# Optimization experiments

Hardware: AMD Instinct MI355X
Metric: run time of the kernel (lower is better)

Reference implementation:

```python
import math
import jax, jax.numpy as jnp
import numpy as np

B, P, L = 32, 128, 64
DIN, TE, H, NH, NL = 16, 64, 512, 8, 2
DH = H // NH
DP = DIN + TE
TAU = 300.0
DELTA = 300.0

_PARAM_SPEC = [
    ("te_scale_w", (1, 1)), ("te_scale_b", (1,)),
    ("te_per_w", (TE - 1, 1)), ("te_per_b", (TE - 1,)),
    ("inp_w", (H, DP)), ("inp_b", (H,)),
    ("wq", (H, H)), ("bq", (H,)), ("wk", (H, H)), ("bk", (H,)),
    ("wv", (H, H)), ("bv", (H,)), ("wo", (H, H)), ("bo", (H,)),
    ("ffn_w1", (H, H)), ("ffn_b1", (H,)), ("ffn_w2", (H, H)), ("ffn_b2", (H,)),
    ("ln1_g", (H,)), ("ln1_b", (H,)), ("ln2_g", (H,)), ("ln2_b", (H,)),
    ("exists_bias", (1, 1, H)),
    ("gwq", (NL, H, H)), ("gbq", (NL, H)), ("gwk", (NL, H, H)), ("gbk", (NL, H)),
    ("gwv", (NL, H, H)), ("gbv", (NL, H)), ("gwo", (NL, H, H)), ("gbo", (NL, H)),
]


def setup_inputs() -> dict:
    key = jax.random.key(0)
    ks = jax.random.split(key, 3 + len(_PARAM_SPEC))
    inp = {
        "x": jax.random.normal(ks[0], (B, P, L, DIN), jnp.float32),
        "tt": jax.random.uniform(ks[1], (B, P, L, 1), jnp.float32),
        "mask": jax.random.randint(ks[2], (B, P, L, 1), 0, 2).astype(jnp.int32),
    }
    for i, (name, shp) in enumerate(_PARAM_SPEC):
        inp[name] = 0.02 * jax.random.normal(ks[3 + i], shp, jnp.float32)
    # LayerNorm affine params: gamma=1, beta=0
    inp["ln1_g"] = jnp.ones((H,), jnp.float32)
    inp["ln1_b"] = jnp.zeros((H,), jnp.float32)
    inp["ln2_g"] = jnp.ones((H,), jnp.float32)
    inp["ln2_b"] = jnp.zeros((H,), jnp.float32)
    return inp


def _layernorm(x, g, b, eps=1e-5):
    m = x.mean(-1, keepdims=True)
    v = ((x - m) ** 2).mean(-1, keepdims=True)
    return (x - m) / jnp.sqrt(v + eps) * g + b


def _time_bias(m):
    idx = jnp.arange(m)
    dist = jnp.abs(idx[:, None] - idx[None, :]).astype(jnp.float32) * DELTA
    return jnp.log(jnp.exp(-dist / TAU) + 1e-12)  # [P, P]


def _pos_encoding(p, d):
    pos = jnp.arange(p, dtype=jnp.float32)[:, None]
    div = jnp.exp(jnp.arange(0, d, 2, dtype=jnp.float32) * (-math.log(10000.0) / d))
    pe = jnp.zeros((p, d), jnp.float32)
    pe = pe.at[:, 0::2].set(jnp.sin(pos * div))
    pe = pe.at[:, 1::2].set(jnp.cos(pos * div))
    return pe


def reference(x, tt, mask,
              te_scale_w, te_scale_b, te_per_w, te_per_b,
              inp_w, inp_b, wq, bq, wk, bk, wv, bv, wo, bo,
              ffn_w1, ffn_b1, ffn_w2, ffn_b2, ln1_g, ln1_b, ln2_g, ln2_b,
              exists_bias, gwq, gbq, gwk, gbk, gwv, gbv, gwo, gbo):
    b, p, l, _ = x.shape
    # --- Learnable time embedding: scale linear + sin(periodic linear), concat ---
    te1 = tt @ te_scale_w.T + te_scale_b                      # [B,P,L,1]
    te2 = jnp.sin(tt @ te_per_w.T + te_per_b)                 # [B,P,L,TE-1]
    pts = jnp.concatenate([x, te1, te2], axis=-1)             # [B,P,L,DP]

    valid = (mask[..., 0] > 0).reshape(b * p, l)              # [N,L] bool
    h = (pts.reshape(b * p, l, DP) @ inp_w.T) + inp_b         # [N,L,H]

    has_any = jnp.any(valid, axis=1)                          # [N]
    key_pad = ~valid
    # Empty patches: unmask position 0 and zero its features
    key_pad = key_pad.at[:, 0].set(key_pad[:, 0] & has_any)
    pos0 = (jnp.arange(l) == 0)[None, :, None]
    h = jnp.where((~has_any)[:, None, None] & pos0, 0.0, h)

    # --- Intra-patch MHA (GAT) ---
    def heads(t, w, bias):
        return ((t @ w.T) + bias).reshape(b * p, l, NH, DH)
    q, k, v = heads(h, wq, bq), heads(h, wk, bk), heads(h, wv, bv)
    sc = jnp.einsum("nqhd,nkhd->nhqk", q, k) / math.sqrt(DH)
    sc = jnp.where(key_pad[:, None, None, :], -1e9, sc)
    z = jnp.einsum("nhqk,nkhd->nqhd", jax.nn.softmax(sc, axis=-1), v)
    z = z.reshape(b * p, l, H) @ wo.T + bo
    h = _layernorm(h + z, ln1_g, ln1_b)
    ffn = jax.nn.relu(h @ ffn_w1.T + ffn_b1) @ ffn_w2.T + ffn_b2
    h = _layernorm(h + ffn, ln2_g, ln2_b)

    # Masked mean pooling -> patch tokens
    w = valid.astype(jnp.float32)[..., None]                  # [N,L,1]
    denom = jnp.clip(w.sum(axis=1), 1.0)
    h = ((h * w).sum(axis=1) / denom).reshape(b, p, H)        # [B,P,H]

    # Exists bias for missing patches + positional encoding
    pexists = has_any.reshape(b, p).astype(jnp.float32)       # [B,P]
    h = h + exists_bias * (1.0 - pexists)[..., None]
    h = h + _pos_encoding(p, H)[None]

    # --- Patch-level time-biased graph attention stack (residual) ---
    tb = _time_bias(p)[None, None]                            # [1,1,P,P]
    kp = (pexists <= 0.0)[:, None, None, :]                   # [B,1,1,P]
    for li in range(NL):
        def gh(t, w, bias):
            return ((t @ w.T) + bias).reshape(b, p, NH, DH)
        q = gh(h, gwq[li], gbq[li])
        k = gh(h, gwk[li], gbk[li])
        v = gh(h, gwv[li], gbv[li])
        att = jnp.einsum("bqhd,bkhd->bhqk", q, k) / math.sqrt(DH) + tb
        att = jnp.where(kp, -1e9, att)
        out = jnp.einsum("bhqk,bkhd->bqhd", jax.nn.softmax(att, axis=-1), v)
        out = out.reshape(b, p, H) @ gwo[li].T + gbo[li]
        out = out * pexists[..., None]
        h = h + out
    return h
```

## Files before the change

kernel.cpp:

```cpp
#include <hip/hip_runtime.h>

#define NTOK 4096
#define CH   512
#define NCHUNK 8

typedef _Float16 f16;
typedef __attribute__((ext_vector_type(8))) _Float16 half8;
typedef __attribute__((ext_vector_type(4))) _Float16 half4;
typedef __attribute__((ext_vector_type(4))) float f32x4;

#define OFF_INPW 0
#define OFF_WQKV (512*128)
#define OFF_WO   (OFF_WQKV + 3*512*512)
#define OFF_W1   (OFF_WO + 512*512)
#define OFF_W2   (OFF_W1 + 512*512)
#define OFF_GW   (OFF_W2 + 512*512)
#define WBF_TOT  (OFF_GW + 8*512*512)

static __device__ __forceinline__ f32x4 mfma16(half8 a, half8 b, f32x4 c){
  return __builtin_amdgcn_mfma_f32_16x16x32_f16(a, b, c, 0, 0, 0);
}

static __device__ __forceinline__ void gld_lds16(const f16* g, f16* l){
  __builtin_amdgcn_global_load_lds(
      (const __attribute__((address_space(1))) void*)g,
      (__attribute__((address_space(3))) void*)l, 16, 0, 0);
}

__global__ __launch_bounds__(256) void conv_weights(
    const float* __restrict__ inpw, const float* __restrict__ wq, const float* __restrict__ wk,
    const float* __restrict__ wv, const float* __restrict__ wo, const float* __restrict__ w1,
    const float* __restrict__ w2, const float* __restrict__ gwq, const float* __restrict__ gwk,
    const float* __restrict__ gwv, const float* __restrict__ gwo, f16* __restrict__ wbf,
    const float* __restrict__ bq, const float* __restrict__ bk, const float* __restrict__ bv,
    const float* __restrict__ gbq, const float* __restrict__ gbk, const float* __restrict__ gbv,
    float* __restrict__ biasb)
{
  int e = blockIdx.x*256 + threadIdx.x;
  int y = blockIdx.y;
  if (y == 0){
    if (e < 512*128){
      int row = e>>7, col = e&127;
      float v = (col < 80) ? inpw[row*80 + col] : 0.f;
      wbf[OFF_INPW + e] = (f16)v;
    }
    return;
  }
  if (y == 15){
    if (e < 1536){
      biasb[e] = (e < 512) ? bq[e] : (e < 1024 ? bk[e-512] : bv[e-1024]);
    } else if (e < 3*1536){
      int idx = e - 1536, li = idx/1536, c = idx - li*1536;
      float v = (c < 512) ? gbq[li*512 + c] : (c < 1024 ? gbk[li*512 + c-512] : gbv[li*512 + c-1024]);
      biasb[e] = v;
    }
    return;
  }
  if (e >= 512*512) return;
  const float* src; int off;
  if (y <= 6){
    const float* tab[6] = {wq, wk, wv, wo, w1, w2};
    src = tab[y-1]; off = OFF_WQKV + (y-1)*512*512;
  } else {
    int idx = y-7; int li = idx>>2, part = idx&3;
    const float* tab[4] = {gwq, gwk, gwv, gwo};
    src = tab[part] + (size_t)li*512*512; off = OFF_GW + idx*512*512;
  }
  wbf[off + e] = (f16)src[e];
}

__global__ __launch_bounds__(256) void build_mask(
    const int* __restrict__ mask, float* __restrict__ mb, float* __restrict__ pex)
{
  int wv = threadIdx.x>>6, lane = threadIdx.x&63;
  int n = blockIdx.x*4 + wv;
  int valid = mask[(size_t)n*64 + lane] > 0;
  unsigned long long ball = __ballot(valid);
  int hasany = (ball != 0ull);
  int masked = (lane == 0) ? (!valid && hasany) : (!valid);
  mb[(size_t)n*64 + lane] = masked ? -1e9f : 0.f;
  if (lane == 0) pex[n] = hasany ? 1.f : 0.f;
}

__global__ __launch_bounds__(256) void pts_build(
    const float* __restrict__ x, const float* __restrict__ tt,
    const float* __restrict__ tsw, const float* __restrict__ tsb,
    const float* __restrict__ tpw, const float* __restrict__ tpb,
    f16* __restrict__ pts, int rowbase)
{
  int e = blockIdx.x*256 + threadIdx.x;
  int r = e>>7, col = e&127;
  size_t grow = (size_t)rowbase + r;
  float v;
  if (col < 16) v = x[grow*16 + col];
  else if (col >= 80) v = 0.f;
  else {
    float t = tt[grow];
    if (col == 16) v = t*tsw[0] + tsb[0];
    else           v = __sinf(t*tpw[col-17] + tpb[col-17]);
  }
  pts[e] = (f16)v;
}

template<int RESID, bool RELU, bool OUTF32, bool ZEMPTY>
__global__ __launch_bounds__(256) void gemm128(
    const f16* __restrict__ A, const f16* __restrict__ W, const float* __restrict__ bias,
    void* __restrict__ Cout, const void* __restrict__ Rsd, const float* __restrict__ pex,
    int K, int lda, int ldc, int nbase)
{
  __shared__ __align__(16) f16 As[128][64];
  __shared__ __align__(16) f16 Bs[128][64];
  const int tid = threadIdx.x;
  const int m0 = blockIdx.x*128, n0 = blockIdx.y*128;
  const int wv = tid>>6, lane = tid&63, l15 = lane&15, quad = lane>>4;
  const int wm = (wv&1)*64, wn = (wv>>1)*64;
  const int srow = lane>>3;
  const int schunk = (lane&7) ^ srow;
  f32x4 acc[4][4] = {};
  for (int kc = 0; kc < K; kc += 64){
    __syncthreads();
    #pragma unroll
    for (int i=0; i<4; i++){
      const int rA = wv*32 + i*8;
      gld_lds16(A + (size_t)(m0 + rA + srow)*lda + kc + schunk*8, &As[rA][0]);
      gld_lds16(W + (size_t)(n0 + rA + srow)*K   + kc + schunk*8, &Bs[rA][0]);
    }
    __syncthreads();
    #pragma unroll
    for (int kk=0; kk<2; kk++){
      half8 av[4], bv8[4];
      #pragma unroll
      for (int t=0; t<4; t++){
        const int ra = wm + t*16 + l15;
        av[t]  = *(const half8*)(&As[ra][(((kk*4 + quad) ^ (ra&7)))*8]);
        const int rb = wn + t*16 + l15;
        bv8[t] = *(const half8*)(&Bs[rb][(((kk*4 + quad) ^ (rb&7)))*8]);
      }
      #pragma unroll
      for (int mt=0; mt<4; mt++)
        #pragma unroll
        for (int nt=0; nt<4; nt++)
          acc[mt][nt] = mfma16(av[mt], bv8[nt], acc[mt][nt]);
    }
  }
  #pragma unroll
  for (int mt=0; mt<4; mt++){
    #pragma unroll
    for (int nt=0; nt<4; nt++){
      #pragma unroll
      for (int i=0; i<4; i++){
        int gr = m0 + wm + mt*16 + quad*4 + i;
        int gc = n0 + wn + nt*16 + l15;
        float v = acc[mt][nt][i] + bias[gc];
        if (RELU) v = fmaxf(v, 0.f);
        if (RESID == 1) v += (float)((const f16*)Rsd)[(size_t)gr*ldc + gc];
        if (ZEMPTY){ if ((gr&63)==0 && pex[nbase + (gr>>6)]==0.f) v = 0.f; }
        if (RESID == 2) v = v*pex[gr] + ((const float*)Rsd)[(size_t)gr*ldc + gc];
        if (OUTF32) ((float*)Cout)[(size_t)gr*ldc + gc] = v;
        else        ((f16*)Cout)[(size_t)gr*ldc + gc] = (f16)v;
      }
    }
  }
}

__global__ __launch_bounds__(128) void attn_patch(
    f16* __restrict__ qkv, const float* __restrict__ maskbias, int nbase)
{
  __shared__ f16 Vt[2][64][72];
  __shared__ f16 Ps[2][64][72];
  __shared__ float mbs[64];
  const int tid = threadIdx.x, wv = tid>>6, lane = tid&63, l15 = lane&15, quad = lane>>4;
  const int n = blockIdx.x, h = blockIdx.y*2 + wv;
  if (tid < 64) mbs[tid] = maskbias[(size_t)(nbase+n)*64 + tid];
  const f16* Vb = qkv + 1024 + h*64;
  for (int i=0; i<64; i++)
    Vt[wv][lane][i] = Vb[((size_t)n*64 + i)*1536 + lane];
  __syncthreads();
  const f16* Qb  = qkv + (size_t)n*64*1536 + h*64;
  const f16* Kbb = Qb + 512;
  f32x4 sacc[4][4] = {};
  #pragma unroll
  for (int kc=0; kc<2; kc++){
    half8 af[4], bf[4];
    #pragma unroll
    for (int t4=0; t4<4; t4++){
      af[t4] = *(const half8*)(Qb  + (size_t)(t4*16 + l15)*1536 + kc*32 + quad*8);
      bf[t4] = *(const half8*)(Kbb + (size_t)(t4*16 + l15)*1536 + kc*32 + quad*8);
    }
    #pragma unroll
    for (int ti=0; ti<4; ti++)
      #pragma unroll
      for (int tj=0; tj<4; tj++)
        sacc[ti][tj] = mfma16(af[ti], bf[tj], sacc[ti][tj]);
  }
  #pragma unroll
  for (int ti=0; ti<4; ti++){
    #pragma unroll
    for (int i=0; i<4; i++){
      float mx = -1e30f;
      #pragma unroll
      for (int tj=0; tj<4; tj++){
        float sv = sacc[ti][tj][i]*0.125f + mbs[tj*16 + l15];
        sacc[ti][tj][i] = sv;
        mx = fmaxf(mx, sv);
      }
      #pragma unroll
      for (int off=1; off<16; off<<=1) mx = fmaxf(mx, __shfl_xor(mx, off, 64));
      float sum = 0.f;
      #pragma unroll
      for (int tj=0; tj<4; tj++){
        float pv = __expf(sacc[ti][tj][i] - mx);
        sacc[ti][tj][i] = pv; sum += pv;
      }
      #pragma unroll
      for (int off=1; off<16; off<<=1) sum += __shfl_xor(sum, off, 64);
      float inv = 1.f/sum;
      int q = ti*16 + quad*4 + i;
      #pragma unroll
      for (int tj=0; tj<4; tj++)
        Ps[wv][q][tj*16 + l15] = (f16)(sacc[ti][tj][i]*inv);
    }
  }
  __syncthreads();
  f32x4 zacc[4][4] = {};
  #pragma unroll
  for (int kc=0; kc<2; kc++){
    half8 va[4], pb[4];
    #pragma unroll
    for (int t4=0; t4<4; t4++){
      va[t4] = *(const half8*)(&Vt[wv][t4*16 + l15][kc*32 + quad*8]);
      pb[t4] = *(const half8*)(&Ps[wv][t4*16 + l15][kc*32 + quad*8]);
    }
    #pragma unroll
    for (int ti2=0; ti2<4; ti2++)
      #pragma unroll
      for (int tj=0; tj<4; tj++)
        zacc[ti2][tj] = mfma16(va[ti2], pb[tj], zacc[ti2][tj]);
  }
  __syncthreads();
  #pragma unroll
  for (int ti2=0; ti2<4; ti2++)
    #pragma unroll
    for (int tj=0; tj<4; tj++){
      int q = tj*16 + l15, d0 = ti2*16 + quad*4;
      half4 pk;
      #pragma unroll
      for (int i=0; i<4; i++) pk[i] = (f16)zacc[ti2][tj][i];
      *(half4*)(&Vt[wv][q][d0]) = pk;
    }
  __syncthreads();
  #pragma unroll
  for (int i=0; i<8; i++){
    int q = i*8 + (lane>>3), d0 = (lane&7)*8;
    *(uint4*)(qkv + ((size_t)n*64 + q)*1536 + h*64 + d0) = *(const uint4*)(&Vt[wv][q][d0]);
  }
}

__global__ __launch_bounds__(256) void ln_rows(
    const f16* __restrict__ X, f16* __restrict__ Y,
    const float* __restrict__ g, const float* __restrict__ b)
{
  int wv = threadIdx.x>>6, lane = threadIdx.x&63;
  size_t row = (size_t)blockIdx.x*4 + wv;
  half8 raw = *(const half8*)(X + row*512 + lane*8);
  float xv[8];
  #pragma unroll
  for (int j=0; j<8; j++) xv[j] = (float)raw[j];
  float s = 0.f;
  #pragma unroll
  for (int j=0; j<8; j++) s += xv[j];
  #pragma unroll
  for (int off=1; off<64; off<<=1) s += __shfl_xor(s, off, 64);
  float mean = s*(1.f/512.f);
  float vs = 0.f;
  #pragma unroll
  for (int j=0; j<8; j++){ float d = xv[j]-mean; vs += d*d; }
  #pragma unroll
  for (int off=1; off<64; off<<=1) vs += __shfl_xor(vs, off, 64);
  float rstd = rsqrtf(vs*(1.f/512.f) + 1e-5f);
  half8 o;
  #pragma unroll
  for (int j=0; j<8; j++){
    int c = lane*8 + j;
    o[j] = (f16)((xv[j]-mean)*rstd*g[c] + b[c]);
  }
  *(half8*)(Y + row*512 + lane*8) = o;
}

__global__ __launch_bounds__(256) void pool_ln2(
    const f16* __restrict__ X, const int* __restrict__ mask,
    const float* __restrict__ g, const float* __restrict__ b, const float* __restrict__ eb,
    float* __restrict__ out, int nbase)
{
  __shared__ float mArr[64], rArr[64], vArr[64];
  const int tid = threadIdx.x, wv = tid>>6, lane = tid&63;
  const int n = blockIdx.x, ng = nbase + n, p = ng & 127;
  for (int j=0; j<16; j++){
    int l = wv*16 + j;
    half8 raw = *(const half8*)(X + ((size_t)n*64 + l)*512 + lane*8);
    float s=0.f, ss=0.f;
    #pragma unroll
    for (int jj=0; jj<8; jj++){ float f = (float)raw[jj]; s += f; ss += f*f; }
    #pragma unroll
    for (int off=1; off<64; off<<=1){ s += __shfl_xor(s, off, 64); ss += __shfl_xor(ss, off, 64); }
    if (lane == 0){
      float m = s*(1.f/512.f);
      mArr[l] = m; rArr[l] = rsqrtf(ss*(1.f/512.f) - m*m + 1e-5f);
    }
  }
  if (tid < 64) vArr[tid] = (mask[(size_t)ng*64 + tid] > 0) ? 1.f : 0.f;
  __syncthreads();
  float cnt = 0.f;
  #pragma unroll
  for (int l=0; l<64; l++) cnt += vArr[l];
  float denom = fmaxf(cnt, 1.f);
  float pexv = cnt > 0.f ? 1.f : 0.f;
  float a0=0.f, a1=0.f;
  for (int l=0; l<64; l++){
    float wgt = vArr[l], m = mArr[l], rs = rArr[l];
    float x0 = (float)X[((size_t)n*64+l)*512 + tid];
    float x1 = (float)X[((size_t)n*64+l)*512 + tid + 256];
    a0 += wgt*(x0-m)*rs; a1 += wgt*(x1-m)*rs;
  }
  #pragma unroll
  for (int k=0; k<2; k++){
    int c = tid + k*256;
    float acc = k ? a1 : a0;
    float fr = __expf(-(float)(c & ~1) * (9.210340371976184f/512.f));
    float ang = (float)p * fr;
    float pe = (c & 1) ? cosf(ang) : sinf(ang);
    float o = (g[c]*acc + b[c]*cnt)/denom + eb[c]*(1.f - pexv) + pe;
    out[(size_t)ng*512 + c] = o;
  }
}

__global__ __launch_bounds__(256) void cvt_f32_f16(const float* __restrict__ s, f16* __restrict__ d){
  int i = blockIdx.x*256 + threadIdx.x;
  d[i] = (f16)s[i];
}

__global__ __launch_bounds__(256) void attn_graph(
    f16* __restrict__ qkv, const float* __restrict__ pexists)
{
  __shared__ f16 Vt[64][136];
  __shared__ f16 Ps[4][32][136];
  __shared__ float pxs[128];
  const int tid = threadIdx.x, wv = tid>>6, lane = tid&63, l15 = lane&15, quad = lane>>4;
  const int b = blockIdx.x, h = blockIdx.y;
  if (tid < 128) pxs[tid] = pexists[b*128 + tid];
  const f16* Vb = qkv + 1024 + h*64;
  for (int i=0; i<32; i++){
    int e = tid + i*256, k = e>>6, d = e&63;
    Vt[d][k] = Vb[((size_t)b*128 + k)*1536 + d];
  }
  __syncthreads();
  const f16* Qb = qkv + h*64;
  const f16* Kb = qkv + 512 + h*64;
  const int qb = wv*32;
  f32x4 sacc[2][8] = {};
  #pragma unroll
  for (int kc=0; kc<2; kc++){
    half8 af[2], bf[8];
    #pragma unroll
    for (int ti=0; ti<2; ti++)
      af[ti] = *(const half8*)(Qb + ((size_t)b*128 + qb + ti*16 + l15)*1536 + kc*32 + quad*8);
    #pragma unroll
    for (int tj=0; tj<8; tj++)
      bf[tj] = *(const half8*)(Kb + ((size_t)b*128 + tj*16 + l15)*1536 + kc*32 + quad*8);
    #pragma unroll
    for (int ti=0; ti<2; ti++)
      #pragma unroll
      for (int tj=0; tj<8; tj++)
        sacc[ti][tj] = mfma16(af[ti], bf[tj], sacc[ti][tj]);
  }
  #pragma unroll
  for (int ti=0; ti<2; ti++){
    #pragma unroll
    for (int i=0; i<4; i++){
      int q = qb + ti*16 + quad*4 + i;
      float mx = -1e30f;
      #pragma unroll
      for (int tj=0; tj<8; tj++){
        int col = tj*16 + l15;
        int dd = q - col; if (dd < 0) dd = -dd;
        float tb = __logf(__expf(-(float)dd) + 1e-12f);
        float sv = sacc[ti][tj][i]*0.125f + tb + (pxs[col] > 0.f ? 0.f : -1e9f);
        sacc[ti][tj][i] = sv;
        mx = fmaxf(mx, sv);
      }
      #pragma unroll
      for (int off=1; off<16; off<<=1) mx = fmaxf(mx, __shfl_xor(mx, off, 64));
      float sum = 0.f;
      #pragma unroll
      for (int tj=0; tj<8; tj++){
        float pv = __expf(sacc[ti][tj][i] - mx);
        sacc[ti][tj][i] = pv; sum += pv;
      }
      #pragma unroll
      for (int off=1; off<16; off<<=1) sum += __shfl_xor(sum, off, 64);
      float inv = 1.f/sum;
      int ql = ti*16 + quad*4 + i;
      #pragma unroll
      for (int tj=0; tj<8; tj++)
        Ps[wv][ql][tj*16 + l15] = (f16)(sacc[ti][tj][i]*inv);
    }
  }
  __syncthreads();
  f32x4 zacc[4][2] = {};
  #pragma unroll
  for (int kc=0; kc<4; kc++){
    half8 va[4], pb[2];
    #pragma unroll
    for (int ti2=0; ti2<4; ti2++)
      va[ti2] = *(const half8*)(&Vt[ti2*16 + l15][kc*32 + quad*8]);
    #pragma unroll
    for (int tjq=0; tjq<2; tjq++)
      pb[tjq] = *(const half8*)(&Ps[wv][tjq*16 + l15][kc*32 + quad*8]);
    #pragma unroll
    for (int ti2=0; ti2<4; ti2++)
      #pragma unroll
      for (int tjq=0; tjq<2; tjq++)
        zacc[ti2][tjq] = mfma16(va[ti2], pb[tjq], zacc[ti2][tjq]);
  }
  __syncthreads();
  #pragma unroll
  for (int ti2=0; ti2<4; ti2++)
    #pragma unroll
    for (int tjq=0; tjq<2; tjq++){
      int ql = tjq*16 + l15, d0 = ti2*16 + quad*4;
      half4 pk;
      #pragma unroll
      for (int i=0; i<4; i++) pk[i] = (f16)zacc[ti2][tjq][i];
      *(half4*)(&Ps[wv][ql][d0]) = pk;
    }
  __syncthreads();
  {
    int q = tid>>1, hf = tid&1;
    const f16* src = &Ps[q>>5][q&31][hf*32];
    #pragma unroll
    for (int j=0; j<4; j++)
      *(uint4*)(qkv + ((size_t)b*128 + q)*1536 + h*64 + hf*32 + j*8) = *(const uint4*)(src + j*8);
  }
}

extern "C" void kernel_launch(void* const* d_in, const int* in_sizes, int n_in,
                              void* d_out, int out_size, void* d_ws, size_t ws_size,
                              hipStream_t stream)
{
  (void)in_sizes; (void)n_in; (void)out_size; (void)ws_size;
  const float* x    = (const float*)d_in[0];
  const float* tt   = (const float*)d_in[1];
  const int*   mask = (const int*)  d_in[2];
  const float* tsw  = (const float*)d_in[3];
  const float* tsb  = (const float*)d_in[4];
  const float* tpw  = (const float*)d_in[5];
  const float* tpb  = (const float*)d_in[6];
  const float* inpw = (const float*)d_in[7];
  const float* inpb = (const float*)d_in[8];
  const float* wq   = (const float*)d_in[9];
  const float* bq   = (const float*)d_in[10];
  const float* wk   = (const float*)d_in[11];
  const float* bk   = (const float*)d_in[12];
  const float* wv   = (const float*)d_in[13];
  const float* bv   = (const float*)d_in[14];
  const float* wo   = (const float*)d_in[15];
  const float* bo   = (const float*)d_in[16];
  const float* w1   = (const float*)d_in[17];
  const float* b1   = (const float*)d_in[18];
  const float* w2   = (const float*)d_in[19];
  const float* b2   = (const float*)d_in[20];
  const float* ln1g = (const float*)d_in[21];
  const float* ln1b = (const float*)d_in[22];
  const float* ln2g = (const float*)d_in[23];
  const float* ln2b = (const float*)d_in[24];
  const float* eb   = (const float*)d_in[25];
  const float* gwq  = (const float*)d_in[26];
  const float* gbq  = (const float*)d_in[27];
  const float* gwk  = (const float*)d_in[28];
  const float* gbk  = (const float*)d_in[29];
  const float* gwv  = (const float*)d_in[30];
  const float* gbv  = (const float*)d_in[31];
  const float* gwo  = (const float*)d_in[32];
  const float* gbo  = (const float*)d_in[33];
  float* out = (float*)d_out;

  char* wp = (char*)d_ws;
  auto alloc = [&](size_t bytes)->char*{
    char* p = wp; wp += (bytes + 255) & ~(size_t)255; return p;
  };
  f16*   wbf   = (f16*)  alloc((size_t)WBF_TOT*2);
  float* mb    = (float*)alloc((size_t)NTOK*64*4);
  float* pex   = (float*)alloc((size_t)NTOK*4);
  float* biasb = (float*)alloc((size_t)3*1536*4);
  f16*   ptsb  = (f16*)  alloc((size_t)CH*64*128*2);
  f16*   bufA  = (f16*)  alloc((size_t)CH*64*512*2);
  f16*   bufB  = (f16*)  alloc((size_t)CH*64*512*2);
  f16*   bufC  = (f16*)  alloc((size_t)CH*64*512*2);
  f16*   qkv   = (f16*)  alloc((size_t)CH*64*1536*2);

  conv_weights<<<dim3(1024,16),256,0,stream>>>(inpw,wq,wk,wv,wo,w1,w2,gwq,gwk,gwv,gwo,wbf,
                                               bq,bk,bv,gbq,gbk,gbv,biasb);
  build_mask<<<NTOK/4,256,0,stream>>>(mask, mb, pex);

  const int MB = CH*64/128;
  for (int ch=0; ch<NCHUNK; ch++){
    int nbase = ch*CH;
    int rowbase = nbase*64;
    pts_build<<<CH*64*128/256,256,0,stream>>>(x,tt,tsw,tsb,tpw,tpb,ptsb,rowbase);
    gemm128<0,false,false,true ><<<dim3(MB,4),256,0,stream>>>(ptsb, wbf+OFF_INPW, inpb, bufA, nullptr, pex, 128, 128, 512, nbase);
    gemm128<0,false,false,false><<<dim3(MB,12),256,0,stream>>>(bufA, wbf+OFF_WQKV, biasb, qkv, nullptr, nullptr, 512, 512, 1536, 0);
    attn_patch<<<dim3(CH,4),128,0,stream>>>(qkv, mb, nbase);
    gemm128<1,false,false,false><<<dim3(MB,4),256,0,stream>>>(qkv, wbf+OFF_WO, bo, bufA, bufA, nullptr, 512, 1536, 512, 0);
    ln_rows<<<CH*64/4,256,0,stream>>>(bufA, bufB, ln1g, ln1b);
    gemm128<0,true ,false,false><<<dim3(MB,4),256,0,stream>>>(bufB, wbf+OFF_W1, b1, bufC, nullptr, nullptr, 512, 512, 512, 0);
    gemm128<1,false,false,false><<<dim3(MB,4),256,0,stream>>>(bufC, wbf+OFF_W2, b2, bufB, bufB, nullptr, 512, 512, 512, 0);
    pool_ln2<<<CH,256,0,stream>>>(bufB, mask, ln2g, ln2b, eb, out, nbase);
  }

  f16* hbf  = bufA;
  f16* qkvg = bufB;
  for (int li=0; li<2; li++){
    cvt_f32_f16<<<NTOK*512/256,256,0,stream>>>(out, hbf);
    gemm128<0,false,false,false><<<dim3(32,12),256,0,stream>>>(hbf, wbf+OFF_GW + (size_t)li*4*512*512, biasb + 1536*(1+li), qkvg, nullptr, nullptr, 512, 512, 1536, 0);
    attn_graph<<<dim3(32,8),256,0,stream>>>(qkvg, pex);
    gemm128<2,false,true ,false><<<dim3(32,4),256,0,stream>>>(qkvg, wbf+OFF_GW + (size_t)(li*4+3)*512*512, gbo+li*512, out, out, pex, 512, 1536, 512, 0);
  }
}
```

Baseline: 2.398 ms.

## Double-buffer GEMM staging, vectorize epilogue via LDS, fuse f16 conversions

The GEMM now double-buffers its LDS tiles, issuing the next K-slice's global-to-LDS loads before computing the current one. Its epilogue stages results through shared memory so that output, residual and pex handling use 16-byte vector accesses. attn_patch loads V with half8 vector reads before transposing it. The standalone f32-to-f16 conversion kernels are removed: pool_ln2 and the first graph output GEMM now write an f16 copy of h directly. Risks include an extra f16 rounding of values before the residual add in the epilogue and higher LDS use per block.

```diff
diff --git a/kernel.cpp b/kernel.cpp
--- a/kernel.cpp
+++ b/kernel.cpp
@@ -102,14 +102,16 @@
   pts[e] = (f16)v;
 }
 
-template<int RESID, bool RELU, bool OUTF32, bool ZEMPTY>
+template<int RESID, bool RELU, bool OUTF32, bool ZEMPTY, bool DUAL>
 __global__ __launch_bounds__(256) void gemm128(
     const f16* __restrict__ A, const f16* __restrict__ W, const float* __restrict__ bias,
     void* __restrict__ Cout, const void* __restrict__ Rsd, const float* __restrict__ pex,
-    int K, int lda, int ldc, int nbase)
-{
-  __shared__ __align__(16) f16 As[128][64];
-  __shared__ __align__(16) f16 Bs[128][64];
+    f16* __restrict__ Cdual, int K, int lda, int ldc, int nbase)
+{
+  __shared__ union {
+    f16 stg[2][2][128][64];
+    f16 cs[128][136];
+  } sm;
   const int tid = threadIdx.x;
   const int m0 = blockIdx.x*128, n0 = blockIdx.y*128;
   const int wv = tid>>6, lane = tid&63, l15 = lane&15, quad = lane>>4;
@@ -117,24 +119,30 @@
   const int srow = lane>>3;
   const int schunk = (lane&7) ^ srow;
   f32x4 acc[4][4] = {};
-  for (int kc = 0; kc < K; kc += 64){
-    __syncthreads();
+
+  auto stage = [&](int kc, int b){
     #pragma unroll
     for (int i=0; i<4; i++){
       const int rA = wv*32 + i*8;
-      gld_lds16(A + (size_t)(m0 + rA + srow)*lda + kc + schunk*8, &As[rA][0]);
-      gld_lds16(W + (size_t)(n0 + rA + srow)*K   + kc + schunk*8, &Bs[rA][0]);
-    }
+      gld_lds16(A + (size_t)(m0 + rA + srow)*lda + kc + schunk*8, &sm.stg[b][0][rA][0]);
+      gld_lds16(W + (size_t)(n0 + rA + srow)*K   + kc + schunk*8, &sm.stg[b][1][rA][0]);
+    }
+  };
+
+  stage(0, 0);
+  int buf = 0;
+  for (int kc = 0; kc < K; kc += 64, buf ^= 1){
     __syncthreads();
+    if (kc + 64 < K) stage(kc + 64, buf^1);
     #pragma unroll
     for (int kk=0; kk<2; kk++){
       half8 av[4], bv8[4];
       #pragma unroll
       for (int t=0; t<4; t++){
         const int ra = wm + t*16 + l15;
-        av[t]  = *(const half8*)(&As[ra][(((kk*4 + quad) ^ (ra&7)))*8]);
+        av[t]  = *(const half8*)(&sm.stg[buf][0][ra][(((kk*4 + quad) ^ (ra&7)))*8]);
         const int rb = wn + t*16 + l15;
-        bv8[t] = *(const half8*)(&Bs[rb][(((kk*4 + quad) ^ (rb&7)))*8]);
+        bv8[t] = *(const half8*)(&sm.stg[buf][1][rb][(((kk*4 + quad) ^ (rb&7)))*8]);
       }
       #pragma unroll
       for (int mt=0; mt<4; mt++)
@@ -143,22 +151,62 @@
           acc[mt][nt] = mfma16(av[mt], bv8[nt], acc[mt][nt]);
     }
   }
-  #pragma unroll
-  for (int mt=0; mt<4; mt++){
-    #pragma unroll
-    for (int nt=0; nt<4; nt++){
+  __syncthreads();
+  #pragma unroll
+  for (int nt=0; nt<4; nt++){
+    const float bz = bias[n0 + wn + nt*16 + l15];
+    #pragma unroll
+    for (int mt=0; mt<4; mt++){
       #pragma unroll
       for (int i=0; i<4; i++){
-        int gr = m0 + wm + mt*16 + quad*4 + i;
-        int gc = n0 + wn + nt*16 + l15;
-        float v = acc[mt][nt][i] + bias[gc];
+        float v = acc[mt][nt][i] + bz;
         if (RELU) v = fmaxf(v, 0.f);
-        if (RESID == 1) v += (float)((const f16*)Rsd)[(size_t)gr*ldc + gc];
-        if (ZEMPTY){ if ((gr&63)==0 && pex[nbase + (gr>>6)]==0.f) v = 0.f; }
-        if (RESID == 2) v = v*pex[gr] + ((const float*)Rsd)[(size_t)gr*ldc + gc];
-        if (OUTF32) ((float*)Cout)[(size_t)gr*ldc + gc] = v;
-        else        ((f16*)Cout)[(size_t)gr*ldc + gc] = (f16)v;
+        sm.cs[wm + mt*16 + quad*4 + i][wn + nt*16 + l15] = (f16)v;
       }
+    }
+  }
+  __syncthreads();
+  const int row = tid>>1, c0 = (tid&1)*64;
+  const int gr = m0 + row;
+  float rowscale = 1.f;
+  bool zrow = false;
+  if (ZEMPTY) zrow = ((gr&63)==0) && (pex[nbase + (gr>>6)] == 0.f);
+  if (RESID == 2) rowscale = pex[gr];
+  #pragma unroll
+  for (int j=0; j<8; j++){
+    const int gc = n0 + c0 + j*8;
+    half8 hv = *(const half8*)(&sm.cs[row][c0 + j*8]);
+    float fv[8];
+    #pragma unroll
+    for (int u=0; u<8; u++) fv[u] = (float)hv[u];
+    if (RESID == 1){
+      half8 rv = *(const half8*)((const f16*)Rsd + (size_t)gr*ldc + gc);
+      #pragma unroll
+      for (int u=0; u<8; u++) fv[u] += (float)rv[u];
+    }
+    if (RESID == 2){
+      #pragma unroll
+      for (int u=0; u<8; u++)
+        fv[u] = fv[u]*rowscale + ((const float*)Rsd)[(size_t)gr*ldc + gc + u];
+    }
+    if (ZEMPTY && zrow){
+      #pragma unroll
+      for (int u=0; u<8; u++) fv[u] = 0.f;
+    }
+    if (OUTF32){
+      #pragma unroll
+      for (int u=0; u<8; u++) ((float*)Cout)[(size_t)gr*ldc + gc + u] = fv[u];
+    } else {
+      half8 ov;
+      #pragma unroll
+      for (int u=0; u<8; u++) ov[u] = (f16)fv[u];
+      *(half8*)((f16*)Cout + (size_t)gr*ldc + gc) = ov;
+    }
+    if (DUAL){
+      half8 ov;
+      #pragma unroll
+      for (int u=0; u<8; u++) ov[u] = (f16)fv[u];
+      *(half8*)(Cdual + (size_t)gr*512 + gc) = ov;
     }
   }
 }
@@ -172,9 +220,14 @@
   const int tid = threadIdx.x, wv = tid>>6, lane = tid&63, l15 = lane&15, quad = lane>>4;
   const int n = blockIdx.x, h = blockIdx.y*2 + wv;
   if (tid < 64) mbs[tid] = maskbias[(size_t)(nbase+n)*64 + tid];
-  const f16* Vb = qkv + 1024 + h*64;
-  for (int i=0; i<64; i++)
-    Vt[wv][lane][i] = Vb[((size_t)n*64 + i)*1536 + lane];
+  const f16* Vbp = qkv + (size_t)n*64*1536 + 1024 + h*64;
+  #pragma unroll
+  for (int i=0; i<8; i++){
+    int key = i*8 + (lane>>3), d0 = (lane&7)*8;
+    half8 vv = *(const half8*)(Vbp + (size_t)key*1536 + d0);
+    #pragma unroll
+    for (int j=0; j<8; j++) Vt[wv][d0+j][key] = vv[j];
+  }
   __syncthreads();
   const f16* Qb  = qkv + (size_t)n*64*1536 + h*64;
   const f16* Kbb = Qb + 512;
@@ -290,7 +343,7 @@
 __global__ __launch_bounds__(256) void pool_ln2(
     const f16* __restrict__ X, const int* __restrict__ mask,
     const float* __restrict__ g, const float* __restrict__ b, const float* __restrict__ eb,
-    float* __restrict__ out, int nbase)
+    float* __restrict__ out, f16* __restrict__ hb, int nbase)
 {
   __shared__ float mArr[64], rArr[64], vArr[64];
   const int tid = threadIdx.x, wv = tid>>6, lane = tid&63;
@@ -331,12 +384,8 @@
     float pe = (c & 1) ? cosf(ang) : sinf(ang);
     float o = (g[c]*acc + b[c]*cnt)/denom + eb[c]*(1.f - pexv) + pe;
     out[(size_t)ng*512 + c] = o;
-  }
-}
-
-__global__ __launch_bounds__(256) void cvt_f32_f16(const float* __restrict__ s, f16* __restrict__ d){
-  int i = blockIdx.x*256 + threadIdx.x;
-  d[i] = (f16)s[i];
+    hb[(size_t)ng*512 + c] = (f16)o;
+  }
 }
 
 __global__ __launch_bounds__(256) void attn_graph(
@@ -492,6 +541,7 @@
   float* mb    = (float*)alloc((size_t)NTOK*64*4);
   float* pex   = (float*)alloc((size_t)NTOK*4);
   float* biasb = (float*)alloc((size_t)3*1536*4);
+  f16*   hbf   = (f16*)  alloc((size_t)NTOK*512*2);
   f16*   ptsb  = (f16*)  alloc((size_t)CH*64*128*2);
   f16*   bufA  = (f16*)  alloc((size_t)CH*64*512*2);
   f16*   bufB  = (f16*)  alloc((size_t)CH*64*512*2);
@@ -507,22 +557,23 @@
     int nbase = ch*CH;
     int rowbase = nbase*64;
     pts_build<<<CH*64*128/256,256,0,stream>>>(x,tt,tsw,tsb,tpw,tpb,ptsb,rowbase);
-    gemm128<0,false,false,true ><<<dim3(MB,4),256,0,stream>>>(ptsb, wbf+OFF_INPW, inpb, bufA, nullptr, pex, 128, 128, 512, nbase);
-    gemm128<0,false,false,false><<<dim3(MB,12),256,0,stream>>>(bufA, wbf+OFF_WQKV, biasb, qkv, nullptr, nullptr, 512, 512, 1536, 0);
+    gemm128<0,false,false,true ,false><<<dim3(MB,4),256,0,stream>>>(ptsb, wbf+OFF_INPW, inpb, bufA, nullptr, pex, nullptr, 128, 128, 512, nbase);
+    gemm128<0,false,false,false,false><<<dim3(MB,12),256,0,stream>>>(bufA, wbf+OFF_WQKV, biasb, qkv, nullptr, nullptr, nullptr, 512, 512, 1536, 0);
     attn_patch<<<dim3(CH,4),128,0,stream>>>(qkv, mb, nbase);
-    gemm128<1,false,false,false><<<dim3(MB,4),256,0,stream>>>(qkv, wbf+OFF_WO, bo, bufA, bufA, nullptr, 512, 1536, 512, 0);
+    gemm128<1,false,false,false,false><<<dim3(MB,4),256,0,stream>>>(qkv, wbf+OFF_WO, bo, bufA, bufA, nullptr, nullptr, 512, 1536, 512, 0);
     ln_rows<<<CH*64/4,256,0,stream>>>(bufA, bufB, ln1g, ln1b);
-    gemm128<0,true ,false,false><<<dim3(MB,4),256,0,stream>>>(bufB, wbf+OFF_W1, b1, bufC, nullptr, nullptr, 512, 512, 512, 0);
-    gemm128<1,false,false,false><<<dim3(MB,4),256,0,stream>>>(bufC, wbf+OFF_W2, b2, bufB, bufB, nullptr, 512, 512, 512, 0);
-    pool_ln2<<<CH,256,0,stream>>>(bufB, mask, ln2g, ln2b, eb, out, nbase);
-  }
-
-  f16* hbf  = bufA;
+    gemm128<0,true ,false,false,false><<<dim3(MB,4),256,0,stream>>>(bufB, wbf+OFF_W1, b1, bufC, nullptr, nullptr, nullptr, 512, 512, 512, 0);
+    gemm128<1,false,false,false,false><<<dim3(MB,4),256,0,stream>>>(bufC, wbf+OFF_W2, b2, bufB, bufB, nullptr, nullptr, 512, 512, 512, 0);
+    pool_ln2<<<CH,256,0,stream>>>(bufB, mask, ln2g, ln2b, eb, out, hbf, nbase);
+  }
+
   f16* qkvg = bufB;
   for (int li=0; li<2; li++){
-    cvt_f32_f16<<<NTOK*512/256,256,0,stream>>>(out, hbf);
-    gemm128<0,false,false,false><<<dim3(32,12),256,0,stream>>>(hbf, wbf+OFF_GW + (size_t)li*4*512*512, biasb + 1536*(1+li), qkvg, nullptr, nullptr, 512, 512, 1536, 0);
+    gemm128<0,false,false,false,false><<<dim3(32,12),256,0,stream>>>(hbf, wbf+OFF_GW + (size_t)li*4*512*512, biasb + 1536*(1+li), qkvg, nullptr, nullptr, nullptr, 512, 512, 1536, 0);
     attn_graph<<<dim3(32,8),256,0,stream>>>(qkvg, pex);
-    gemm128<2,false,true ,false><<<dim3(32,4),256,0,stream>>>(qkvg, wbf+OFF_GW + (size_t)(li*4+3)*512*512, gbo+li*512, out, out, pex, 512, 1536, 512, 0);
-  }
-}
+    if (li == 0)
+      gemm128<2,false,true ,false,true ><<<dim3(32,4),256,0,stream>>>(qkvg, wbf+OFF_GW + (size_t)(li*4+3)*512*512, gbo+li*512, out, out, pex, hbf, 512, 1536, 512, 0);
+    else
+      gemm128<2,false,true ,false,false><<<dim3(32,4),256,0,stream>>>(qkvg, wbf+OFF_GW + (size_t)(li*4+3)*512*512, gbo+li*512, out, out, pex, nullptr, 512, 1536, 512, 0);
+  }
+}
```

Result: slower. 2.619 ms (+9.2%).
